# Performance work log

Hardware: AMD Instinct MI355X
Metric: run time of the kernel (lower is better)

Reference implementation:

```python
import jax, jax.numpy as jnp
import numpy as np


def _orth(key, shape):
    # orthogonal init like nn.init.orthogonal_
    a = jax.random.normal(key, shape, dtype=jnp.float32)
    q, r = jnp.linalg.qr(a if shape[0] >= shape[1] else a.T)
    q = q * jnp.sign(jnp.diag(r))
    return q if shape[0] >= shape[1] else q.T


def setup_inputs() -> dict:
    S, B, D, H, M = 512, 128, 256, 512, 16
    key = jax.random.key(0)
    ks = jax.random.split(key, 20)
    inp = {
        "x": jax.random.normal(ks[0], (S, B, D), dtype=jnp.float32),
        "h0": jax.random.normal(ks[1], (B, H), dtype=jnp.float32),
        "c0": jax.random.normal(ks[2], (B, H), dtype=jnp.float32),
        "alpha": jax.random.uniform(ks[3], (B, M * M), dtype=jnp.float32),
        "beta": jax.random.uniform(ks[4], (B, M * M), dtype=jnp.float32),
        "theta": jax.random.uniform(ks[5], (B, M), dtype=jnp.float32),
        "tspan": jax.random.uniform(ks[6], (B,), dtype=jnp.float32),
        "A_mdhp": _orth(ks[7], (M * M, H)),
        "B_mdhp": _orth(ks[8], (M * M, H)),
        "C_mdhp": _orth(ks[9], (M, H)),
        "W_i": _orth(ks[10], (D, H)), "U_i": _orth(ks[11], (H, H)), "b_i": jnp.zeros((H,), jnp.float32),
        "W_f": _orth(ks[12], (D, H)), "U_f": _orth(ks[13], (H, H)), "b_f": jnp.zeros((H,), jnp.float32),
        "W_c": _orth(ks[14], (D, H)), "U_c": _orth(ks[15], (H, H)), "b_c": jnp.zeros((H,), jnp.float32),
        "W_o": _orth(ks[16], (D, H)), "U_o": _orth(ks[17], (H, H)), "b_o": jnp.zeros((H,), jnp.float32),
    }
    return inp


def reference(x, h0, c0, alpha, beta, theta, tspan,
              A_mdhp, B_mdhp, C_mdhp,
              W_i, U_i, b_i, W_f, U_f, b_f, W_c, U_c, b_c, W_o, U_o, b_o):
    # mdhp gate is loop-invariant in the original code; hoist it (same math).
    mdhp = jnp.tanh(alpha @ A_mdhp - (beta * tspan[:, None]) @ B_mdhp + theta @ C_mdhp)  # [B,H]
    # Fuse the four input projections into one big GEMM over all timesteps.
    W = jnp.concatenate([W_i, W_f, W_c, W_o], axis=1)   # [D,4H]
    U = jnp.concatenate([U_i, U_f, U_c, U_o], axis=1)   # [H,4H]
    b = jnp.concatenate([b_i, b_f, b_c, b_o], axis=0)   # [4H]
    xW = jnp.einsum("sbd,dg->sbg", x, W) + b            # [S,B,4H]
    H = h0.shape[-1]

    def step(carry, xw_t):
        h, c = carry
        g = xw_t + h @ U                                # [B,4H]
        i_t = jax.nn.sigmoid(g[:, 0 * H:1 * H])
        f_t = jax.nn.sigmoid(g[:, 1 * H:2 * H])
        c_hat = jnp.tanh(g[:, 2 * H:3 * H])
        o_t = jax.nn.sigmoid(g[:, 3 * H:4 * H])
        c = mdhp * (f_t * c + i_t * c_hat)
        h = o_t * jnp.tanh(c)
        return (h, c), h

    (h_T, c_T), outputs = jax.lax.scan(step, (h0, c0), xW)
    return outputs, (h_T, c_T)
```

## Files before the change

### kernel.cpp

```cpp
#include <hip/hip_runtime.h>
#include <cstdint>
#include <cstddef>


typedef __attribute__((ext_vector_type(8))) short short8;
typedef __attribute__((ext_vector_type(4))) float floatx4;

#define SEQ 512
#define BATCH 128
#define DIN 256
#define HID 512
#define KTOT 768
#define NCHAIN 8
#define NCOLW 32
#define BS_STRIDE 776

__device__ __forceinline__ short f2bf(float f) {
  union { float f; unsigned u; } v; v.f = f;
  unsigned u = v.u + 0x7fffu + ((v.u >> 16) & 1u);
  return (short)(u >> 16);
}
__device__ __forceinline__ float fsig(float x) {
  return 1.f / (1.f + __expf(-x));
}
__device__ __forceinline__ float ftanh(float x) {
  float a = fabsf(x);
  float e = __expf(-2.f * a);
  float r = (1.f - e) / (1.f + e);
  return copysignf(r, x);
}

__device__ __forceinline__ int l2_add_ret(int* p, int v) {
  int old;
  asm volatile("global_atomic_add %0, %1, %2, off sc0\n\t"
               "s_waitcnt vmcnt(0)"
               : "=v"(old)
               : "v"((unsigned long long)(uintptr_t)p), "v"(v)
               : "memory");
  return old;
}
__device__ __forceinline__ void l2_add(int* p, int v) {
  asm volatile("global_atomic_add %0, %1, off"
               :: "v"((unsigned long long)(uintptr_t)p), "v"(v)
               : "memory");
}

__global__ void prep_gt(const float* __restrict__ Wi, const float* __restrict__ Ui,
                        const float* __restrict__ Wf, const float* __restrict__ Uf,
                        const float* __restrict__ Wc, const float* __restrict__ Uc,
                        const float* __restrict__ Wo, const float* __restrict__ Uo,
                        short* __restrict__ GT) {
  int idx = blockIdx.x * 256 + threadIdx.x;
  if (idx >= 2048 * KTOT) return;
  int n = idx / KTOT, k = idx % KTOT;
  int g = n >> 9, hc = n & 511;
  const float* W; const float* U;
  if (g == 0)      { W = Wi; U = Ui; }
  else if (g == 1) { W = Wf; U = Uf; }
  else if (g == 2) { W = Wc; U = Uc; }
  else             { W = Wo; U = Uo; }
  float v = (k < DIN) ? W[k * HID + hc] : U[(k - DIN) * HID + hc];
  GT[idx] = f2bf(v);
}

__global__ void prep_xb(const float* __restrict__ x, short* __restrict__ xb) {
  int idx = blockIdx.x * 256 + threadIdx.x;
  float4 v = ((const float4*)x)[idx];
  short4 o; o.x = f2bf(v.x); o.y = f2bf(v.y); o.z = f2bf(v.z); o.w = f2bf(v.w);
  ((short4*)xb)[idx] = o;
}

__global__ void prep_h0(const float* __restrict__ h0, short* __restrict__ hbuf) {
  int idx = blockIdx.x * 256 + threadIdx.x;
  hbuf[idx] = f2bf(h0[idx]);
}

__global__ void prep_mdhp(const float* __restrict__ alpha, const float* __restrict__ beta,
                          const float* __restrict__ theta, const float* __restrict__ tspan,
                          const float* __restrict__ A, const float* __restrict__ Bm,
                          const float* __restrict__ C, float* __restrict__ mdhp) {
  int idx = blockIdx.x * 256 + threadIdx.x;
  int b = idx >> 9, h = idx & 511;
  float ts = tspan[b];
  float acc = 0.f;
  for (int k = 0; k < 256; ++k)
    acc += alpha[b * 256 + k] * A[k * HID + h] - ts * beta[b * 256 + k] * Bm[k * HID + h];
  for (int k = 0; k < 16; ++k)
    acc += theta[b * 16 + k] * C[k * HID + h];
  mdhp[idx] = tanhf(acc);
}

__global__ void zero_sync(int* __restrict__ cnt, int* __restrict__ cnt2,
                          unsigned* __restrict__ det) {
  int idx = blockIdx.x * 256 + threadIdx.x;
  if (idx < NCHAIN * SEQ) { cnt[idx] = 0; cnt2[idx] = 0; }
  if (idx < 264) det[idx] = 0;
}

__global__ __launch_bounds__(256, 1) void lstm_persist(
    const short* __restrict__ xb, const float* __restrict__ c0,
    const float* __restrict__ bi, const float* __restrict__ bf_,
    const float* __restrict__ bc, const float* __restrict__ bo,
    const short* __restrict__ GT, const float* __restrict__ mdhp,
    int* cnt, int* cnt2, unsigned* det, short* hbuf, float* out) {
  __shared__ __align__(16) short Bs[64 * BS_STRIDE];
  __shared__ float gbuf[2][4][16][17];
  __shared__ int wv[SEQ];
  __shared__ int ready;
  __shared__ int s_mode;

  const int tid = threadIdx.x;
  const int wg = blockIdx.x;
  const int chain = wg & 7;
  const int j = wg >> 3;

  for (int idx = tid; idx < 64 * 384; idx += 256) {
    int lr = idx / 384, dw = idx % 384;
    int n = ((lr >> 4) << 9) + (j << 4) + (lr & 15);
    ((int*)Bs)[lr * 388 + dw] = ((const int*)GT)[n * 384 + dw];
  }
  for (int i = tid; i < SEQ; i += 256) wv[i] = 0;
  if (tid == 0) ready = 0;

  const int er = tid >> 4, ec = tid & 15;
  const int brow = (chain << 4) + er, hcol = (j << 4) + ec;
  float creg = c0[brow * HID + hcol];
  const float mdv = mdhp[brow * HID + hcol];
  const float b0 = bi[hcol], b1 = bf_[hcol], b2 = bc[hcol], b3 = bo[hcol];

  unsigned xid;
  asm volatile("s_getreg_b32 %0, hwreg(HW_REG_XCC_ID)" : "=s"(xid));
  xid &= 15u;
  if (tid == 0) {
    __hip_atomic_store(&det[wg], xid, __ATOMIC_RELAXED, __HIP_MEMORY_SCOPE_AGENT);
    __hip_atomic_fetch_add((int*)&det[256 + chain], 1, __ATOMIC_RELEASE,
                           __HIP_MEMORY_SCOPE_AGENT);
    while (__hip_atomic_load((int*)&det[256 + chain], __ATOMIC_ACQUIRE,
                             __HIP_MEMORY_SCOPE_AGENT) < NCOLW)
      __builtin_amdgcn_s_sleep(2);
    unsigned x0 = __hip_atomic_load(&det[chain], __ATOMIC_RELAXED,
                                    __HIP_MEMORY_SCOPE_AGENT);
    int ok = 1;
    for (int jj = 1; jj < NCOLW; ++jj)
      ok &= (__hip_atomic_load(&det[chain + 8 * jj], __ATOMIC_RELAXED,
                               __HIP_MEMORY_SCOPE_AGENT) == x0);
    s_mode = ok;
  }
  __syncthreads();
  const bool xloc = (s_mode != 0);

  const int lane = tid & 63;
  const int g = tid >> 6;
  const int mr = lane & 15;
  const int q = lane >> 4;
  const int bglob = (chain << 4) + mr;
  const short* Brow = &Bs[(g * 16 + mr) * BS_STRIDE + q * 8];
  int* mycnt = cnt + chain * SEQ;
  int* mycnt2 = cnt2 + chain * SEQ;
  bool esc = false;

  for (int t = 0; t < SEQ; ++t) {
    const short* xr = xb + ((size_t)t * BATCH + bglob) * DIN + q * 8;
    short8 xaf[8];
#pragma unroll
    for (int kk = 0; kk < 8; ++kk) xaf[kk] = *(const short8*)(xr + kk * 32);

    if (t > 0) {
      if (tid == 0) {
        int sp = 0;
        for (;;) {
          int v;
          if (xloc && !esc)
            v = l2_add_ret(&mycnt[t - 1], 0);
          else
            v = __hip_atomic_load(&mycnt2[t - 1], __ATOMIC_RELAXED,
                                  __HIP_MEMORY_SCOPE_AGENT);
          if (v >= NCOLW) break;
          __builtin_amdgcn_s_sleep(1);
          if (++sp > 4000) esc = true;
        }
        __hip_atomic_store(&ready, t, __ATOMIC_RELEASE,
                           __HIP_MEMORY_SCOPE_WORKGROUP);
      }
      while (__hip_atomic_load(&ready, __ATOMIC_ACQUIRE,
                               __HIP_MEMORY_SCOPE_WORKGROUP) < t) {}
      __builtin_amdgcn_sched_barrier(0);
    }

    const short* hr = hbuf + ((size_t)t * BATCH + bglob) * HID + q * 8;
    short8 haf[16];
#pragma unroll
    for (int kk = 0; kk < 16; ++kk) haf[kk] = *(const short8*)(hr + kk * 32);

    floatx4 ax  = {0.f, 0.f, 0.f, 0.f};
    floatx4 ah0 = {0.f, 0.f, 0.f, 0.f};
    floatx4 ah1 = {0.f, 0.f, 0.f, 0.f};

#pragma unroll
    for (int kk = 0; kk < 8; ++kk)
      ax = __builtin_amdgcn_mfma_f32_16x16x32_bf16(
          xaf[kk], *(const short8*)(Brow + kk * 32), ax, 0, 0, 0);

    asm volatile("s_waitcnt vmcnt(0)" ::: "memory");
    __builtin_amdgcn_sched_barrier(0);

#pragma unroll
    for (int kk = 0; kk < 8; ++kk) {
      ah0 = __builtin_amdgcn_mfma_f32_16x16x32_bf16(
          haf[kk], *(const short8*)(Brow + DIN + kk * 32), ah0, 0, 0, 0);
      ah1 = __builtin_amdgcn_mfma_f32_16x16x32_bf16(
          haf[8 + kk], *(const short8*)(Brow + DIN + (8 + kk) * 32), ah1, 0, 0, 0);
    }

    const int p = t & 1;
#pragma unroll
    for (int i = 0; i < 4; ++i)
      gbuf[p][g][q * 4 + i][mr] = ax[i] + ah0[i] + ah1[i];
    __syncthreads();
    {
      float gi = gbuf[p][0][er][ec] + b0;
      float gf = gbuf[p][1][er][ec] + b1;
      float gc = gbuf[p][2][er][ec] + b2;
      float go = gbuf[p][3][er][ec] + b3;
      float it = fsig(gi), ft = fsig(gf), ot = fsig(go);
      float ch = ftanh(gc);
      float cn = mdv * (ft * creg + it * ch);
      creg = cn;
      float hv = ot * ftanh(cn);

      if (t < SEQ - 1) {
        unsigned hb = (unsigned)(unsigned short)f2bf(hv);
        unsigned other = (unsigned)__shfl_xor((int)hb, 1, 64);
        if ((tid & 1) == 0) {
          unsigned pack = hb | (other << 16);
          size_t hidx = ((size_t)(t + 1) * BATCH + brow) * HID + hcol;
          if (xloc)
            *(unsigned*)&hbuf[hidx] = pack;
          else
            __hip_atomic_store((unsigned*)&hbuf[hidx], pack, __ATOMIC_RELAXED,
                               __HIP_MEMORY_SCOPE_AGENT);
        }
      }

      size_t oidx = ((size_t)t * BATCH + brow) * HID + hcol;
      out[oidx] = hv;
      if (t == SEQ - 1) {
        size_t base = (size_t)SEQ * BATCH * HID;
        int e = brow * HID + hcol;
        out[base + e] = hv;
        out[base + BATCH * HID + e] = cn;
      }
    }

    if (t < SEQ - 1) {
      asm volatile("s_waitcnt vmcnt(0)" ::: "memory");
      if (lane == 0) {
        int old = __hip_atomic_fetch_add(&wv[t], 1, __ATOMIC_RELAXED,
                                         __HIP_MEMORY_SCOPE_WORKGROUP);
        if (old == 3) {
          if (xloc) {
            l2_add(&mycnt[t], 1);
            __hip_atomic_fetch_add(&mycnt2[t], 1, __ATOMIC_RELAXED,
                                   __HIP_MEMORY_SCOPE_AGENT);
          } else {
            __hip_atomic_fetch_add(&mycnt2[t], 1, __ATOMIC_RELEASE,
                                   __HIP_MEMORY_SCOPE_AGENT);
          }
        }
      }
    }
  }
}

extern "C" void kernel_launch(void* const* d_in, const int* in_sizes, int n_in,
                              void* d_out, int out_size, void* d_ws, size_t ws_size,
                              hipStream_t stream) {
  const float* x     = (const float*)d_in[0];
  const float* h0    = (const float*)d_in[1];
  const float* c0    = (const float*)d_in[2];
  const float* alpha = (const float*)d_in[3];
  const float* beta  = (const float*)d_in[4];
  const float* theta = (const float*)d_in[5];
  const float* tspan = (const float*)d_in[6];
  const float* Amd   = (const float*)d_in[7];
  const float* Bmd   = (const float*)d_in[8];
  const float* Cmd   = (const float*)d_in[9];
  const float* Wi = (const float*)d_in[10]; const float* Ui = (const float*)d_in[11];
  const float* bi = (const float*)d_in[12];
  const float* Wf = (const float*)d_in[13]; const float* Uf = (const float*)d_in[14];
  const float* bf_ = (const float*)d_in[15];
  const float* Wc = (const float*)d_in[16]; const float* Uc = (const float*)d_in[17];
  const float* bc = (const float*)d_in[18];
  const float* Wo = (const float*)d_in[19]; const float* Uo = (const float*)d_in[20];
  const float* bo = (const float*)d_in[21];

  float* out = (float*)d_out;
  char* ws = (char*)d_ws;
  short* GT     = (short*)ws;
  float* mdhp   = (float*)(ws + 3145728);
  int*   cnt    = (int*)(ws + 3407872);
  int*   cnt2   = (int*)(ws + 3424256);
  unsigned* det = (unsigned*)(ws + 3440640);
  short* xb     = (short*)(ws + 3444736);
  short* hbuf   = (short*)(ws + 36999168);

  zero_sync<<<16, 256, 0, stream>>>(cnt, cnt2, det);
  prep_gt<<<(2048 * KTOT + 255) / 256, 256, 0, stream>>>(Wi, Ui, Wf, Uf, Wc, Uc, Wo, Uo, GT);
  prep_xb<<<16384, 256, 0, stream>>>(x, xb);
  prep_h0<<<256, 256, 0, stream>>>(h0, hbuf);
  prep_mdhp<<<256, 256, 0, stream>>>(alpha, beta, theta, tspan, Amd, Bmd, Cmd, mdhp);
  lstm_persist<<<NCHAIN * NCOLW, 256, 0, stream>>>(xb, c0, bi, bf_, bc, bo,
                                                   GT, mdhp, cnt, cnt2, det, hbuf, out);
}
```

Measured before the change: 2.404 ms.

## Replace counter-based step barrier with NaN-sentinel polling on h buffer

Removes the per-step counter spin on L2 atomics plus the workgroup ready flag. The h buffer is now prefilled with an all-ones sentinel, and every wave polls its own h slice with sc0 loads until no sentinel remains. It keeps a fallback that waits on an agent-scope counter when the chain's workgroups are not all on one XCC. This cuts a round trip between the flag and the data load, at the cost of a full-buffer fill kernel and repeated 16-load polls from every wave, which adds memory traffic. It also relies on no real bf16 pair equalling 0xFFFFFFFF, and on the data being visible without a release fence.

```diff
diff --git a/kernel.cpp b/kernel.cpp
--- a/kernel.cpp
+++ b/kernel.cpp
@@ -29,20 +29,72 @@
   float r = (1.f - e) / (1.f + e);
   return copysignf(r, x);
 }
-
-__device__ __forceinline__ int l2_add_ret(int* p, int v) {
-  int old;
-  asm volatile("global_atomic_add %0, %1, %2, off sc0\n\t"
-               "s_waitcnt vmcnt(0)"
-               : "=v"(old)
-               : "v"((unsigned long long)(uintptr_t)p), "v"(v)
-               : "memory");
-  return old;
-}
-__device__ __forceinline__ void l2_add(int* p, int v) {
-  asm volatile("global_atomic_add %0, %1, off"
-               :: "v"((unsigned long long)(uintptr_t)p), "v"(v)
-               : "memory");
+__device__ __forceinline__ unsigned umax2(unsigned a, unsigned b) {
+  return a > b ? a : b;
+}
+
+__device__ __forceinline__ void hload16_sc0(const short* hr, short8 (&haf)[16]) {
+  asm volatile(
+      "global_load_dwordx4 %0,  %16, off sc0\n\t"
+      "global_load_dwordx4 %1,  %16, off offset:64 sc0\n\t"
+      "global_load_dwordx4 %2,  %16, off offset:128 sc0\n\t"
+      "global_load_dwordx4 %3,  %16, off offset:192 sc0\n\t"
+      "global_load_dwordx4 %4,  %16, off offset:256 sc0\n\t"
+      "global_load_dwordx4 %5,  %16, off offset:320 sc0\n\t"
+      "global_load_dwordx4 %6,  %16, off offset:384 sc0\n\t"
+      "global_load_dwordx4 %7,  %16, off offset:448 sc0\n\t"
+      "global_load_dwordx4 %8,  %16, off offset:512 sc0\n\t"
+      "global_load_dwordx4 %9,  %16, off offset:576 sc0\n\t"
+      "global_load_dwordx4 %10, %16, off offset:640 sc0\n\t"
+      "global_load_dwordx4 %11, %16, off offset:704 sc0\n\t"
+      "global_load_dwordx4 %12, %16, off offset:768 sc0\n\t"
+      "global_load_dwordx4 %13, %16, off offset:832 sc0\n\t"
+      "global_load_dwordx4 %14, %16, off offset:896 sc0\n\t"
+      "global_load_dwordx4 %15, %16, off offset:960 sc0\n\t"
+      "s_waitcnt vmcnt(0)"
+      : "=v"(haf[0]), "=v"(haf[1]), "=v"(haf[2]), "=v"(haf[3]),
+        "=v"(haf[4]), "=v"(haf[5]), "=v"(haf[6]), "=v"(haf[7]),
+        "=v"(haf[8]), "=v"(haf[9]), "=v"(haf[10]), "=v"(haf[11]),
+        "=v"(haf[12]), "=v"(haf[13]), "=v"(haf[14]), "=v"(haf[15])
+      : "v"((unsigned long long)(uintptr_t)hr)
+      : "memory");
+}
+__device__ __forceinline__ void hload16_bypass(const short* hr, short8 (&haf)[16]) {
+  asm volatile(
+      "global_load_dwordx4 %0,  %16, off sc0 sc1\n\t"
+      "global_load_dwordx4 %1,  %16, off offset:64 sc0 sc1\n\t"
+      "global_load_dwordx4 %2,  %16, off offset:128 sc0 sc1\n\t"
+      "global_load_dwordx4 %3,  %16, off offset:192 sc0 sc1\n\t"
+      "global_load_dwordx4 %4,  %16, off offset:256 sc0 sc1\n\t"
+      "global_load_dwordx4 %5,  %16, off offset:320 sc0 sc1\n\t"
+      "global_load_dwordx4 %6,  %16, off offset:384 sc0 sc1\n\t"
+      "global_load_dwordx4 %7,  %16, off offset:448 sc0 sc1\n\t"
+      "global_load_dwordx4 %8,  %16, off offset:512 sc0 sc1\n\t"
+      "global_load_dwordx4 %9,  %16, off offset:576 sc0 sc1\n\t"
+      "global_load_dwordx4 %10, %16, off offset:640 sc0 sc1\n\t"
+      "global_load_dwordx4 %11, %16, off offset:704 sc0 sc1\n\t"
+      "global_load_dwordx4 %12, %16, off offset:768 sc0 sc1\n\t"
+      "global_load_dwordx4 %13, %16, off offset:832 sc0 sc1\n\t"
+      "global_load_dwordx4 %14, %16, off offset:896 sc0 sc1\n\t"
+      "global_load_dwordx4 %15, %16, off offset:960 sc0 sc1\n\t"
+      "s_waitcnt vmcnt(0)"
+      : "=v"(haf[0]), "=v"(haf[1]), "=v"(haf[2]), "=v"(haf[3]),
+        "=v"(haf[4]), "=v"(haf[5]), "=v"(haf[6]), "=v"(haf[7]),
+        "=v"(haf[8]), "=v"(haf[9]), "=v"(haf[10]), "=v"(haf[11]),
+        "=v"(haf[12]), "=v"(haf[13]), "=v"(haf[14]), "=v"(haf[15])
+      : "v"((unsigned long long)(uintptr_t)hr)
+      : "memory");
+}
+
+__device__ __forceinline__ unsigned nan_max(const short8 (&haf)[16]) {
+  unsigned m = 0;
+#pragma unroll
+  for (int kk = 0; kk < 16; ++kk) {
+    unsigned w[4];
+    __builtin_memcpy(w, &haf[kk], 16);
+    m = umax2(m, umax2(umax2(w[0], w[1]), umax2(w[2], w[3])));
+  }
+  return m;
 }
 
 __global__ void prep_gt(const float* __restrict__ Wi, const float* __restrict__ Ui,
@@ -70,6 +122,12 @@
   ((short4*)xb)[idx] = o;
 }
 
+__global__ void fill_nan(uint4* __restrict__ hb) {
+  int idx = blockIdx.x * 256 + threadIdx.x;
+  uint4 v; v.x = 0xFFFFFFFFu; v.y = 0xFFFFFFFFu; v.z = 0xFFFFFFFFu; v.w = 0xFFFFFFFFu;
+  hb[idx] = v;
+}
+
 __global__ void prep_h0(const float* __restrict__ h0, short* __restrict__ hbuf) {
   int idx = blockIdx.x * 256 + threadIdx.x;
   hbuf[idx] = f2bf(h0[idx]);
@@ -90,10 +148,9 @@
   mdhp[idx] = tanhf(acc);
 }
 
-__global__ void zero_sync(int* __restrict__ cnt, int* __restrict__ cnt2,
-                          unsigned* __restrict__ det) {
-  int idx = blockIdx.x * 256 + threadIdx.x;
-  if (idx < NCHAIN * SEQ) { cnt[idx] = 0; cnt2[idx] = 0; }
+__global__ void zero_sync(int* __restrict__ cnt2, unsigned* __restrict__ det) {
+  int idx = blockIdx.x * 256 + threadIdx.x;
+  if (idx < NCHAIN * SEQ) cnt2[idx] = 0;
   if (idx < 264) det[idx] = 0;
 }
 
@@ -102,11 +159,10 @@
     const float* __restrict__ bi, const float* __restrict__ bf_,
     const float* __restrict__ bc, const float* __restrict__ bo,
     const short* __restrict__ GT, const float* __restrict__ mdhp,
-    int* cnt, int* cnt2, unsigned* det, short* hbuf, float* out) {
+    int* cnt2, unsigned* det, short* hbuf, float* out) {
   __shared__ __align__(16) short Bs[64 * BS_STRIDE];
   __shared__ float gbuf[2][4][16][17];
   __shared__ int wv[SEQ];
-  __shared__ int ready;
   __shared__ int s_mode;
 
   const int tid = threadIdx.x;
@@ -120,7 +176,6 @@
     ((int*)Bs)[lr * 388 + dw] = ((const int*)GT)[n * 384 + dw];
   }
   for (int i = tid; i < SEQ; i += 256) wv[i] = 0;
-  if (tid == 0) ready = 0;
 
   const int er = tid >> 4, ec = tid & 15;
   const int brow = (chain << 4) + er, hcol = (j << 4) + ec;
@@ -155,9 +210,8 @@
   const int q = lane >> 4;
   const int bglob = (chain << 4) + mr;
   const short* Brow = &Bs[(g * 16 + mr) * BS_STRIDE + q * 8];
-  int* mycnt = cnt + chain * SEQ;
   int* mycnt2 = cnt2 + chain * SEQ;
-  bool esc = false;
+  bool esc = !xloc;
 
   for (int t = 0; t < SEQ; ++t) {
     const short* xr = xb + ((size_t)t * BATCH + bglob) * DIN + q * 8;
@@ -165,32 +219,30 @@
 #pragma unroll
     for (int kk = 0; kk < 8; ++kk) xaf[kk] = *(const short8*)(xr + kk * 32);
 
-    if (t > 0) {
-      if (tid == 0) {
-        int sp = 0;
-        for (;;) {
-          int v;
-          if (xloc && !esc)
-            v = l2_add_ret(&mycnt[t - 1], 0);
-          else
-            v = __hip_atomic_load(&mycnt2[t - 1], __ATOMIC_RELAXED,
-                                  __HIP_MEMORY_SCOPE_AGENT);
-          if (v >= NCOLW) break;
-          __builtin_amdgcn_s_sleep(1);
-          if (++sp > 4000) esc = true;
-        }
-        __hip_atomic_store(&ready, t, __ATOMIC_RELEASE,
-                           __HIP_MEMORY_SCOPE_WORKGROUP);
-      }
-      while (__hip_atomic_load(&ready, __ATOMIC_ACQUIRE,
-                               __HIP_MEMORY_SCOPE_WORKGROUP) < t) {}
-      __builtin_amdgcn_sched_barrier(0);
-    }
-
     const short* hr = hbuf + ((size_t)t * BATCH + bglob) * HID + q * 8;
     short8 haf[16];
-#pragma unroll
-    for (int kk = 0; kk < 16; ++kk) haf[kk] = *(const short8*)(hr + kk * 32);
+    int att = 0;
+    for (;;) {
+      if (!esc) {
+        hload16_sc0(hr, haf);
+        if (!__any(nan_max(haf) == 0xFFFFFFFFu)) break;
+        if (++att > 20000) esc = true;
+      } else {
+        if (t > 0) {
+          while (__hip_atomic_load(&mycnt2[t - 1], __ATOMIC_RELAXED,
+                                   __HIP_MEMORY_SCOPE_AGENT) < NCOLW)
+            __builtin_amdgcn_s_sleep(1);
+        }
+        if (xloc) {
+          hload16_sc0(hr, haf);
+          if (!__any(nan_max(haf) == 0xFFFFFFFFu)) break;
+        } else {
+          hload16_bypass(hr, haf);
+          break;
+        }
+      }
+    }
+    __builtin_amdgcn_sched_barrier(0);
 
     floatx4 ax  = {0.f, 0.f, 0.f, 0.f};
     floatx4 ah0 = {0.f, 0.f, 0.f, 0.f};
@@ -200,9 +252,6 @@
     for (int kk = 0; kk < 8; ++kk)
       ax = __builtin_amdgcn_mfma_f32_16x16x32_bf16(
           xaf[kk], *(const short8*)(Brow + kk * 32), ax, 0, 0, 0);
-
-    asm volatile("s_waitcnt vmcnt(0)" ::: "memory");
-    __builtin_amdgcn_sched_barrier(0);
 
 #pragma unroll
     for (int kk = 0; kk < 8; ++kk) {
@@ -257,16 +306,9 @@
       if (lane == 0) {
         int old = __hip_atomic_fetch_add(&wv[t], 1, __ATOMIC_RELAXED,
                                          __HIP_MEMORY_SCOPE_WORKGROUP);
-        if (old == 3) {
-          if (xloc) {
-            l2_add(&mycnt[t], 1);
-            __hip_atomic_fetch_add(&mycnt2[t], 1, __ATOMIC_RELAXED,
-                                   __HIP_MEMORY_SCOPE_AGENT);
-          } else {
-            __hip_atomic_fetch_add(&mycnt2[t], 1, __ATOMIC_RELEASE,
-                                   __HIP_MEMORY_SCOPE_AGENT);
-          }
-        }
+        if (old == 3)
+          __hip_atomic_fetch_add(&mycnt2[t], 1, __ATOMIC_RELAXED,
+                                 __HIP_MEMORY_SCOPE_AGENT);
       }
     }
   }
@@ -298,17 +340,17 @@
   char* ws = (char*)d_ws;
   short* GT     = (short*)ws;
   float* mdhp   = (float*)(ws + 3145728);
-  int*   cnt    = (int*)(ws + 3407872);
-  int*   cnt2   = (int*)(ws + 3424256);
-  unsigned* det = (unsigned*)(ws + 3440640);
-  short* xb     = (short*)(ws + 3444736);
-  short* hbuf   = (short*)(ws + 36999168);
-
-  zero_sync<<<16, 256, 0, stream>>>(cnt, cnt2, det);
+  int*   cnt2   = (int*)(ws + 3407872);
+  unsigned* det = (unsigned*)(ws + 3424256);
+  short* xb     = (short*)(ws + 3428352);
+  short* hbuf   = (short*)(ws + 36982784);
+
+  zero_sync<<<16, 256, 0, stream>>>(cnt2, det);
   prep_gt<<<(2048 * KTOT + 255) / 256, 256, 0, stream>>>(Wi, Ui, Wf, Uf, Wc, Uc, Wo, Uo, GT);
+  fill_nan<<<16384, 256, 0, stream>>>((uint4*)hbuf);
   prep_xb<<<16384, 256, 0, stream>>>(x, xb);
   prep_h0<<<256, 256, 0, stream>>>(h0, hbuf);
   prep_mdhp<<<256, 256, 0, stream>>>(alpha, beta, theta, tspan, Amd, Bmd, Cmd, mdhp);
   lstm_persist<<<NCHAIN * NCOLW, 256, 0, stream>>>(xb, c0, bi, bf_, bc, bo,
-                                                   GT, mdhp, cnt, cnt2, det, hbuf, out);
-}
+                                                   GT, mdhp, cnt2, det, hbuf, out);
+}
```

New measurement: 2.331 ms. 3.0% less time.
